# Kernel tuning notes

Hardware: AMD Instinct MI355X
Metric: run time of the kernel (lower is better)

Reference implementation:

```python
import jax, jax.numpy as jnp
import numpy as np

N = 50000      # nodes
E = 800000     # edges (avg degree 16)
C_IN = 256
C_OUT = 256
H = 4
D = C_OUT // H  # 64
NEG_SLOPE = 0.2


def setup_inputs() -> dict:
    key = jax.random.key(0)
    ks = jax.random.split(key, 12)
    glorot = lambda k, shape: jax.random.uniform(k, shape, jnp.float32, -1.0, 1.0) * np.sqrt(6.0 / (shape[0] + shape[1]))
    return {
        "x": jax.random.normal(ks[0], (N, C_IN), jnp.float32),
        "src": jax.random.randint(ks[1], (E,), 0, N, jnp.int32),
        "dst": jax.random.randint(ks[2], (E,), 0, N, jnp.int32),
        "Wl": glorot(ks[3], (C_IN, C_OUT)),
        "bl": jnp.zeros((C_OUT,), jnp.float32),
        "Wr": glorot(ks[4], (C_IN, C_OUT)),
        "br": jnp.zeros((C_OUT,), jnp.float32),
        "Wv": glorot(ks[5], (C_IN, C_OUT)),
        "bv": jnp.zeros((C_OUT,), jnp.float32),
        "att_l": jax.random.normal(ks[6], (1, H, D), jnp.float32) * 0.1,
        "att_r": jax.random.normal(ks[7], (1, H, D), jnp.float32) * 0.1,
    }


def reference(x, src, dst, Wl, bl, Wr, br, Wv, bv, att_l, att_r):
    # lambda_policy=None, gcn_mode=False -> lmbda = lmbda2 = 1.0
    n = x.shape[0]
    sl = ((x @ Wl + bl).reshape(n, H, D) * att_l).sum(-1, keepdims=True)  # [N,H,1]
    sr = ((x @ Wr + br).reshape(n, H, D) * att_r).sum(-1, keepdims=True)  # [N,H,1]
    xv = (x @ Wv + bv).reshape(n, H, D)                                    # [N,H,D]

    # --- convolve branch: average scores over in-neighborhood (incl. self) ---
    hlr = jnp.concatenate([sl, sr], axis=1)                   # [N,2H,1]
    conv = jax.ops.segment_sum(hlr[src], dst, num_segments=n)  # sum_{u->v} hsrc[u]
    deg = jax.ops.segment_sum(jnp.ones((src.shape[0],), x.dtype), dst, num_segments=n)
    agg = (hlr + conv) / (1.0 + deg[:, None, None])            # [N,2H,1]
    sl, sr = agg[:, :H], agg[:, H:]

    # --- edge attention: gather-add-leakyrelu, segment softmax over dst ---
    e = jax.nn.leaky_relu(sl[src] + sr[dst], NEG_SLOPE)        # [E,H,1]
    emax = jax.ops.segment_max(e, dst, num_segments=n)
    emax = jnp.where(jnp.isfinite(emax), emax, 0.0)
    ex = jnp.exp(e - emax[dst])
    denom = jax.ops.segment_sum(ex, dst, num_segments=n)
    a = ex / jnp.maximum(denom[dst], 1e-16)                    # [E,H,1]

    # --- weighted message aggregation ---
    out = jax.ops.segment_sum(xv[src] * a, dst, num_segments=n)  # [N,H,D]
    return out
```

## Files before the change

kernel.cpp:

```cpp
#include <hip/hip_runtime.h>

#define C_IN 256
#define C_OUT 256
#define NH 4
#define HD 64
#define NEG_SLOPE 0.2f

typedef _Float16 half8 __attribute__((ext_vector_type(8)));
typedef _Float16 half4v __attribute__((ext_vector_type(4)));
typedef float floatx4 __attribute__((ext_vector_type(4)));

__global__ void make_eff_w(const float* __restrict__ Wl, const float* __restrict__ Wr,
                           const float* __restrict__ bl, const float* __restrict__ br,
                           const float* __restrict__ attl, const float* __restrict__ attr,
                           float* __restrict__ Ws, float* __restrict__ bs)
{
    int c = blockIdx.x;
    int t = threadIdx.x;
    int h = t >> 6, d = t & 63;
    float al = attl[t], ar = attr[t];
    float vl, vr;
    if (c < C_IN) { vl = Wl[c * C_OUT + t] * al; vr = Wr[c * C_OUT + t] * ar; }
    else          { vl = bl[t] * al;             vr = br[t] * ar; }
#pragma unroll
    for (int off = 32; off >= 1; off >>= 1) {
        vl += __shfl_xor(vl, off, 64);
        vr += __shfl_xor(vr, off, 64);
    }
    if (d == 0) {
        if (c < C_IN) { Ws[c * 8 + h] = vl; Ws[c * 8 + 4 + h] = vr; }
        else          { bs[h] = vl;         bs[4 + h] = vr; }
    }
}

__global__ void transpose_w(const float* __restrict__ Wv, _Float16* __restrict__ WvT)
{
    int idx = blockIdx.x * 256 + threadIdx.x;
    int n = idx >> 8, k = idx & 255;
    WvT[n * 256 + k] = (_Float16)Wv[k * 256 + n];
}

__global__ __launch_bounds__(256) void node_scores(const float* __restrict__ x,
    const float* __restrict__ Ws, const float* __restrict__ bs,
    float* __restrict__ s, int N)
{
    int lane = threadIdx.x & 63, wid = threadIdx.x >> 6;
    float w[4][8];
#pragma unroll
    for (int i = 0; i < 4; ++i)
#pragma unroll
        for (int jq = 0; jq < 2; ++jq) {
            float4 v = *(const float4*)(Ws + (4 * lane + i) * 8 + jq * 4);
            w[i][jq * 4 + 0] = v.x; w[i][jq * 4 + 1] = v.y;
            w[i][jq * 4 + 2] = v.z; w[i][jq * 4 + 3] = v.w;
        }
    float b0[8];
#pragma unroll
    for (int j = 0; j < 8; ++j) b0[j] = bs[j];

    int wglob = blockIdx.x * 4 + wid;
    int nwaves = gridDim.x * 4;
    for (int n = wglob; n < N; n += nwaves) {
        float4 xv4 = *(const float4*)(x + (size_t)n * 256 + 4 * lane);
        float acc[8];
#pragma unroll
        for (int j = 0; j < 8; ++j)
            acc[j] = xv4.x * w[0][j] + xv4.y * w[1][j] + xv4.z * w[2][j] + xv4.w * w[3][j];
#pragma unroll
        for (int off = 32; off >= 1; off >>= 1)
#pragma unroll
            for (int j = 0; j < 8; ++j) acc[j] += __shfl_xor(acc[j], off, 64);
        if (lane == 0) {
            *(float4*)(s + (size_t)n * 8)     = make_float4(acc[0] + b0[0], acc[1] + b0[1], acc[2] + b0[2], acc[3] + b0[3]);
            *(float4*)(s + (size_t)n * 8 + 4) = make_float4(acc[4] + b0[4], acc[5] + b0[5], acc[6] + b0[6], acc[7] + b0[7]);
        }
    }
}

__global__ __launch_bounds__(256) void gemm_xv(const float* __restrict__ x,
    const _Float16* __restrict__ WvT, const float* __restrict__ bv,
    _Float16* __restrict__ xv, int M)
{
    __shared__ __align__(16) _Float16 As[128][40];
    __shared__ __align__(16) _Float16 Bs[128][40];
    int tid = threadIdx.x;
    int wid = tid >> 6, lane = tid & 63;
    int quad = lane >> 4, r16 = lane & 15;
    int m0 = blockIdx.x * 128, n0 = blockIdx.y * 128;

    floatx4 acc[2][8];
#pragma unroll
    for (int i = 0; i < 2; ++i)
#pragma unroll
        for (int j = 0; j < 8; ++j) acc[i][j] = (floatx4){0.f, 0.f, 0.f, 0.f};

    int arow = tid >> 3, af4 = tid & 7;
    int brow = tid >> 2, bg  = tid & 3;

    for (int k0 = 0; k0 < 256; k0 += 32) {
#pragma unroll
        for (int p = 0; p < 4; ++p) {
            int rr = arow + p * 32;
            int gm = m0 + rr;
            float4 v = make_float4(0.f, 0.f, 0.f, 0.f);
            if (gm < M) v = *(const float4*)(x + (size_t)gm * 256 + k0 + af4 * 4);
            _Float16* dp = &As[rr][af4 * 4];
            dp[0] = (_Float16)v.x; dp[1] = (_Float16)v.y;
            dp[2] = (_Float16)v.z; dp[3] = (_Float16)v.w;
        }
#pragma unroll
        for (int p = 0; p < 2; ++p) {
            int nr = brow + p * 64;
            *(float4*)&Bs[nr][bg * 8] = *(const float4*)(WvT + (size_t)(n0 + nr) * 256 + k0 + bg * 8);
        }
        __syncthreads();
        half8 a[2], b[8];
#pragma unroll
        for (int rg = 0; rg < 2; ++rg)
            a[rg] = *(const half8*)&As[wid * 32 + rg * 16 + r16][quad * 8];
#pragma unroll
        for (int cg = 0; cg < 8; ++cg)
            b[cg] = *(const half8*)&Bs[cg * 16 + r16][quad * 8];
#pragma unroll
        for (int rg = 0; rg < 2; ++rg)
#pragma unroll
            for (int cg = 0; cg < 8; ++cg)
                acc[rg][cg] = __builtin_amdgcn_mfma_f32_16x16x32_f16(a[rg], b[cg], acc[rg][cg], 0, 0, 0);
        __syncthreads();
    }
#pragma unroll
    for (int rg = 0; rg < 2; ++rg) {
        int rbase = m0 + wid * 32 + rg * 16 + quad * 4;
#pragma unroll
        for (int cg = 0; cg < 8; ++cg) {
            int gcol = n0 + cg * 16 + r16;
            float bias = bv[gcol];
#pragma unroll
            for (int rr = 0; rr < 4; ++rr) {
                int grow = rbase + rr;
                if (grow < M)
                    xv[(size_t)grow * 256 + gcol] = (_Float16)(acc[rg][cg][rr] + bias);
            }
        }
    }
}

__global__ void deg_kernel(const int* __restrict__ dst, int* __restrict__ deg, int E)
{
    int i = blockIdx.x * 256 + threadIdx.x;
    if (i < E) atomicAdd(&deg[dst[i]], 1);
}

__global__ void scan_part(const int* __restrict__ deg, int* __restrict__ partials,
                          int N, int chunk)
{
    __shared__ int sd[256];
    int b = blockIdx.x, t = threadIdx.x;
    int idx = b * chunk + t;
    int v = (t < chunk && idx < N) ? deg[idx] : 0;
    sd[t] = v; __syncthreads();
    for (int off = 128; off >= 1; off >>= 1) {
        if (t < off) sd[t] += sd[t + off];
        __syncthreads();
    }
    if (t == 0) partials[b] = sd[0];
}

__global__ void scan_partials(const int* __restrict__ partials, int* __restrict__ pscan)
{
    __shared__ int sd[256];
    int t = threadIdx.x;
    int v = partials[t];
    sd[t] = v; __syncthreads();
    for (int off = 1; off < 256; off <<= 1) {
        int x = (t >= off) ? sd[t - off] : 0;
        __syncthreads();
        sd[t] += x;
        __syncthreads();
    }
    pscan[t] = sd[t] - v;
}

__global__ void scan_final(const int* __restrict__ deg, const int* __restrict__ pscan,
                           int* __restrict__ offs, int N, int chunk)
{
    __shared__ int sd[256];
    int b = blockIdx.x, t = threadIdx.x;
    int idx = b * chunk + t;
    int v = (t < chunk && idx < N) ? deg[idx] : 0;
    sd[t] = v; __syncthreads();
    for (int off = 1; off < 256; off <<= 1) {
        int x = (t >= off) ? sd[t - off] : 0;
        __syncthreads();
        sd[t] += x;
        __syncthreads();
    }
    int incl = sd[t], excl = incl - v;
    int base = pscan[b];
    if (t < chunk && idx < N) offs[idx] = base + excl;
    if (idx == N - 1) offs[N] = base + incl;
}

__global__ void scatter_kernel(const int* __restrict__ src, const int* __restrict__ dst,
                               const int* __restrict__ offs, int* __restrict__ cursor,
                               int* __restrict__ csr_src, int E)
{
    int i = blockIdx.x * 256 + threadIdx.x;
    if (i < E) {
        int d = dst[i];
        int p = offs[d] + atomicAdd(&cursor[d], 1);
        csr_src[p] = src[i];
    }
}

__global__ void agg_kernel(const float* __restrict__ s, const int* __restrict__ csr_src,
                           const int* __restrict__ offs, const int* __restrict__ deg,
                           float* __restrict__ aggl, float* __restrict__ aggr, int N)
{
    int gid = blockIdx.x * 256 + threadIdx.x;
    int n = gid >> 3, c = gid & 7;
    if (n >= N) return;
    int off = offs[n], dg = deg[n];
    float acc = s[(size_t)n * 8 + c];
    int i = 0;
    for (; i + 4 <= dg; i += 4) {
        int p0 = csr_src[off + i];
        int p1 = csr_src[off + i + 1];
        int p2 = csr_src[off + i + 2];
        int p3 = csr_src[off + i + 3];
        float v0 = s[(size_t)p0 * 8 + c];
        float v1 = s[(size_t)p1 * 8 + c];
        float v2 = s[(size_t)p2 * 8 + c];
        float v3 = s[(size_t)p3 * 8 + c];
        acc += (v0 + v1) + (v2 + v3);
    }
    for (; i < dg; ++i) acc += s[(size_t)csr_src[off + i] * 8 + c];
    acc *= 1.0f / (1.0f + (float)dg);
    if (c < 4) aggl[(size_t)n * 4 + c]     = acc;
    else       aggr[(size_t)n * 4 + c - 4] = acc;
}

__global__ __launch_bounds__(256) void attn_out(const float* __restrict__ aggl,
    const float* __restrict__ aggr, const int* __restrict__ csr_src,
    const int* __restrict__ offs, const int* __restrict__ deg,
    const _Float16* __restrict__ xv, float* __restrict__ out, int N)
{
    int wid = threadIdx.x >> 6, lane = threadIdx.x & 63;
    int myhead = lane >> 4, myedge = lane & 15, grp = lane & 48;
    int nwaves = gridDim.x * 4;

    for (int n = blockIdx.x * 4 + wid; n < N; n += nwaves) {
        int off = offs[n], dg = deg[n];
        float ar = aggr[(unsigned)(n * 4 + myhead)];

        float denom = 0.f, o0 = 0.f, o1 = 0.f, o2 = 0.f, o3 = 0.f;

        int cs = 0; float wexp = 0.f;
        if (myedge < dg) {
            cs = csr_src[off + myedge];
            float e = aggl[(unsigned)((cs << 2) + myhead)] + ar;
            e = (e > 0.f) ? e : NEG_SLOPE * e;
            wexp = __expf(e);
        }

        for (int b = 0; b < dg; b += 16) {
            int   cs_c = cs;
            float w_c  = wexp;
            cs = 0; wexp = 0.f;
            int nb = b + 16;
            if (nb + myedge < dg) {
                cs = csr_src[off + nb + myedge];
                float e = aggl[(unsigned)((cs << 2) + myhead)] + ar;
                e = (e > 0.f) ? e : NEG_SLOPE * e;
                wexp = __expf(e);
            }
            denom += w_c;
#pragma unroll
            for (int j = 0; j < 16; ++j) {
                int   sidx = __shfl(cs_c, j, 64);
                float w    = __shfl(w_c, grp + j, 64);
                const half4v hv = *(const half4v*)(xv + (unsigned)((sidx << 8) | (lane << 2)));
                o0 += w * (float)hv[0];
                o1 += w * (float)hv[1];
                o2 += w * (float)hv[2];
                o3 += w * (float)hv[3];
            }
        }

#pragma unroll
        for (int o = 1; o <= 8; o <<= 1) denom += __shfl_xor(denom, o, 64);
        float inv = 1.0f / fmaxf(denom, 1e-16f);
        floatx4 res = {o0 * inv, o1 * inv, o2 * inv, o3 * inv};
        __builtin_nontemporal_store(res, (floatx4*)(out + (size_t)n * 256 + (lane << 2)));
    }
}

extern "C" void kernel_launch(void* const* d_in, const int* in_sizes, int n_in,
                              void* d_out, int out_size, void* d_ws, size_t ws_size,
                              hipStream_t stream)
{
    const float* x    = (const float*)d_in[0];
    const int*   src  = (const int*)d_in[1];
    const int*   dst  = (const int*)d_in[2];
    const float* Wl   = (const float*)d_in[3];
    const float* bl   = (const float*)d_in[4];
    const float* Wr   = (const float*)d_in[5];
    const float* br   = (const float*)d_in[6];
    const float* Wv   = (const float*)d_in[7];
    const float* bv   = (const float*)d_in[8];
    const float* attl = (const float*)d_in[9];
    const float* attr = (const float*)d_in[10];
    float* out = (float*)d_out;

    int N = in_sizes[0] / C_IN;
    int E = in_sizes[1];

    char* p = (char*)d_ws;
    auto alloc = [&](size_t bytes) -> void* {
        uintptr_t q = (uintptr_t)p;
        q = (q + 255) & ~(uintptr_t)255;
        p = (char*)(q + bytes);
        return (void*)q;
    };
    float* Ws     = (float*)alloc((size_t)C_IN * 8 * sizeof(float));
    float* bs     = (float*)alloc(8 * sizeof(float));
    float* s      = (float*)alloc((size_t)N * 8 * sizeof(float));
    float* aggl   = (float*)alloc((size_t)N * 4 * sizeof(float));
    float* aggr   = (float*)alloc((size_t)N * 4 * sizeof(float));
    int* deg      = (int*)alloc((size_t)N * sizeof(int));
    int* offs     = (int*)alloc((size_t)(N + 1) * sizeof(int));
    int* cursor   = (int*)alloc((size_t)N * sizeof(int));
    int* partials = (int*)alloc(256 * sizeof(int));
    int* pscan    = (int*)alloc(256 * sizeof(int));
    int* csr_src  = (int*)alloc((size_t)E * sizeof(int));
    _Float16* WvT = (_Float16*)alloc((size_t)C_IN * C_OUT * sizeof(_Float16));
    _Float16* xv  = (_Float16*)alloc((size_t)N * C_OUT * sizeof(_Float16));

    hipMemsetAsync(deg, 0, (size_t)N * sizeof(int), stream);
    hipMemsetAsync(cursor, 0, (size_t)N * sizeof(int), stream);

    make_eff_w<<<C_IN + 1, 256, 0, stream>>>(Wl, Wr, bl, br, attl, attr, Ws, bs);
    transpose_w<<<(C_IN * C_OUT) / 256, 256, 0, stream>>>(Wv, WvT);
    node_scores<<<768, 256, 0, stream>>>(x, Ws, bs, s, N);
    gemm_xv<<<dim3((N + 127) / 128, C_OUT / 128), 256, 0, stream>>>(x, WvT, bv, xv, N);
    deg_kernel<<<(E + 255) / 256, 256, 0, stream>>>(dst, deg, E);
    int chunk = (N + 255) / 256;
    scan_part<<<256, 256, 0, stream>>>(deg, partials, N, chunk);
    scan_partials<<<1, 256, 0, stream>>>(partials, pscan);
    scan_final<<<256, 256, 0, stream>>>(deg, pscan, offs, N, chunk);
    scatter_kernel<<<(E + 255) / 256, 256, 0, stream>>>(src, dst, offs, cursor, csr_src, E);
    agg_kernel<<<(N * 8 + 255) / 256, 256, 0, stream>>>(s, csr_src, offs, deg, aggl, aggr, N);
    attn_out<<<2048, 256, 0, stream>>>(aggl, aggr, csr_src, offs, deg, xv, out, N);
}
```

Before: 351.0 us.

## Split wave into two edge halves with 16-byte xv gathers in attention kernel

The attention/aggregation kernel now has each half-wave process alternating edges, with every lane loading 8 fp16 features (16 bytes) per gather instead of 4. The two halves' partial sums are combined with a cross-half shuffle before the store. The grid-stride loop and next-batch prefetch are replaced by one wave per node launched over N/4 blocks. The GEMM staging also writes the converted fp16 values as one vector store. The aim is wider memory transactions and fewer loop iterations for the gather-bound step, at the cost of losing the software prefetch and issuing a larger grid.

```diff
diff --git a/kernel.cpp b/kernel.cpp
--- a/kernel.cpp
+++ b/kernel.cpp
@@ -104,9 +104,10 @@
             int gm = m0 + rr;
             float4 v = make_float4(0.f, 0.f, 0.f, 0.f);
             if (gm < M) v = *(const float4*)(x + (size_t)gm * 256 + k0 + af4 * 4);
-            _Float16* dp = &As[rr][af4 * 4];
-            dp[0] = (_Float16)v.x; dp[1] = (_Float16)v.y;
-            dp[2] = (_Float16)v.z; dp[3] = (_Float16)v.w;
+            half4v tmp;
+            tmp[0] = (_Float16)v.x; tmp[1] = (_Float16)v.y;
+            tmp[2] = (_Float16)v.z; tmp[3] = (_Float16)v.w;
+            *(half4v*)&As[rr][af4 * 4] = tmp;
         }
 #pragma unroll
         for (int p = 0; p < 2; ++p) {
@@ -246,52 +247,59 @@
     const _Float16* __restrict__ xv, float* __restrict__ out, int N)
 {
     int wid = threadIdx.x >> 6, lane = threadIdx.x & 63;
-    int myhead = lane >> 4, myedge = lane & 15, grp = lane & 48;
-    int nwaves = gridDim.x * 4;
-
-    for (int n = blockIdx.x * 4 + wid; n < N; n += nwaves) {
-        int off = offs[n], dg = deg[n];
-        float ar = aggr[(unsigned)(n * 4 + myhead)];
-
-        float denom = 0.f, o0 = 0.f, o1 = 0.f, o2 = 0.f, o3 = 0.f;
-
+    int n = blockIdx.x * 4 + wid;
+    if (n >= N) return;
+    int myhead = lane >> 4, myedge = lane & 15;
+    int ehalf = lane >> 5;
+    int cgrp  = lane & 31;
+    int wbase = ((lane & 24) << 1) + ehalf;
+    int off = offs[n], dg = deg[n];
+    float ar = aggr[(unsigned)(n * 4 + myhead)];
+
+    float denom = 0.f;
+    float o[8] = {0.f, 0.f, 0.f, 0.f, 0.f, 0.f, 0.f, 0.f};
+
+    for (int b = 0; b < dg; b += 16) {
+        int rem = dg - b;
+        int cnt = rem < 16 ? rem : 16;
         int cs = 0; float wexp = 0.f;
-        if (myedge < dg) {
-            cs = csr_src[off + myedge];
+        if (myedge < cnt) {
+            cs = csr_src[off + b + myedge];
             float e = aggl[(unsigned)((cs << 2) + myhead)] + ar;
             e = (e > 0.f) ? e : NEG_SLOPE * e;
             wexp = __expf(e);
         }
-
-        for (int b = 0; b < dg; b += 16) {
-            int   cs_c = cs;
-            float w_c  = wexp;
-            cs = 0; wexp = 0.f;
-            int nb = b + 16;
-            if (nb + myedge < dg) {
-                cs = csr_src[off + nb + myedge];
-                float e = aggl[(unsigned)((cs << 2) + myhead)] + ar;
-                e = (e > 0.f) ? e : NEG_SLOPE * e;
-                wexp = __expf(e);
+        denom += wexp;
+        if (cnt == 16) {
+#pragma unroll
+            for (int j = 0; j < 16; j += 2) {
+                int   sidx = __shfl(cs, j + ehalf, 64);
+                float w    = __shfl(wexp, wbase + j, 64);
+                const half8 hv = *(const half8*)(xv + (unsigned)((sidx << 8) + (cgrp << 3)));
+#pragma unroll
+                for (int k = 0; k < 8; ++k) o[k] += w * (float)hv[k];
             }
-            denom += w_c;
-#pragma unroll
-            for (int j = 0; j < 16; ++j) {
-                int   sidx = __shfl(cs_c, j, 64);
-                float w    = __shfl(w_c, grp + j, 64);
-                const half4v hv = *(const half4v*)(xv + (unsigned)((sidx << 8) | (lane << 2)));
-                o0 += w * (float)hv[0];
-                o1 += w * (float)hv[1];
-                o2 += w * (float)hv[2];
-                o3 += w * (float)hv[3];
+        } else {
+            for (int j = 0; j < cnt; j += 2) {
+                int   sidx = __shfl(cs, j + ehalf, 64);
+                float w    = __shfl(wexp, wbase + j, 64);
+                const half8 hv = *(const half8*)(xv + (unsigned)((sidx << 8) + (cgrp << 3)));
+#pragma unroll
+                for (int k = 0; k < 8; ++k) o[k] += w * (float)hv[k];
             }
         }
-
-#pragma unroll
-        for (int o = 1; o <= 8; o <<= 1) denom += __shfl_xor(denom, o, 64);
-        float inv = 1.0f / fmaxf(denom, 1e-16f);
-        floatx4 res = {o0 * inv, o1 * inv, o2 * inv, o3 * inv};
-        __builtin_nontemporal_store(res, (floatx4*)(out + (size_t)n * 256 + (lane << 2)));
+    }
+
+#pragma unroll
+    for (int o2 = 1; o2 <= 8; o2 <<= 1) denom += __shfl_xor(denom, o2, 64);
+    float dh = __shfl(denom, ((lane >> 3) & 3) << 4, 64);
+    float inv = 1.0f / fmaxf(dh, 1e-16f);
+#pragma unroll
+    for (int k = 0; k < 8; ++k) { o[k] += __shfl_xor(o[k], 32, 64); o[k] *= inv; }
+    if (lane < 32) {
+        float* op = out + (size_t)n * 256 + (cgrp << 3);
+        *(float4*)op       = make_float4(o[0], o[1], o[2], o[3]);
+        *(float4*)(op + 4) = make_float4(o[4], o[5], o[6], o[7]);
     }
 }
 
@@ -350,5 +358,5 @@
     scan_final<<<256, 256, 0, stream>>>(deg, pscan, offs, N, chunk);
     scatter_kernel<<<(E + 255) / 256, 256, 0, stream>>>(src, dst, offs, cursor, csr_src, E);
     agg_kernel<<<(N * 8 + 255) / 256, 256, 0, stream>>>(s, csr_src, offs, deg, aggl, aggr, N);
-    attn_out<<<2048, 256, 0, stream>>>(aggl, aggr, csr_src, offs, deg, xv, out, N);
-}
+    attn_out<<<(N + 3) / 4, 256, 0, stream>>>(aggl, aggr, csr_src, offs, deg, xv, out, N);
+}
```

New measurement: 350.0 us. Within noise of the previous version (-0.3%).

## Skip padded gathers in attention aggregation and launch one wave per node

Applied to the files above, without the earlier changes.

The attention-output kernel now gathers only as many neighbor rows as the node actually has. It does this by splitting each 16-edge chunk into power-of-two sub-blocks, where before it always ran the full 16 gathers and multiplied the padded ones by zero weight. The grid-stride loop is replaced with one wave per node, and the first 64 edges' indices, scores and exponentials are all loaded up front to raise memory-level parallelism. The GEMM staging also writes the four fp16 values as a single vector store. The trade-off is more branching and register pressure, and more blocks to launch.

```diff
diff --git a/kernel.cpp b/kernel.cpp
--- a/kernel.cpp
+++ b/kernel.cpp
@@ -104,9 +104,10 @@
             int gm = m0 + rr;
             float4 v = make_float4(0.f, 0.f, 0.f, 0.f);
             if (gm < M) v = *(const float4*)(x + (size_t)gm * 256 + k0 + af4 * 4);
-            _Float16* dp = &As[rr][af4 * 4];
-            dp[0] = (_Float16)v.x; dp[1] = (_Float16)v.y;
-            dp[2] = (_Float16)v.z; dp[3] = (_Float16)v.w;
+            half4v tmp;
+            tmp[0] = (_Float16)v.x; tmp[1] = (_Float16)v.y;
+            tmp[2] = (_Float16)v.z; tmp[3] = (_Float16)v.w;
+            *(half4v*)&As[rr][af4 * 4] = tmp;
         }
 #pragma unroll
         for (int p = 0; p < 2; ++p) {
@@ -240,59 +241,100 @@
     else       aggr[(size_t)n * 4 + c - 4] = acc;
 }
 
+template<int SZ>
+__device__ __forceinline__ void gather_sub(int cs, float w, int base, int grp, int lane,
+    const _Float16* __restrict__ xv,
+    float& o0, float& o1, float& o2, float& o3)
+{
+#pragma unroll
+    for (int j = 0; j < SZ; ++j) {
+        int   sidx = __shfl(cs, base + j, 64);
+        float wv   = __shfl(w, grp + base + j, 64);
+        const half4v hv = *(const half4v*)(xv + (unsigned)((sidx << 8) | (lane << 2)));
+        o0 += wv * (float)hv[0];
+        o1 += wv * (float)hv[1];
+        o2 += wv * (float)hv[2];
+        o3 += wv * (float)hv[3];
+    }
+}
+
+__device__ __forceinline__ void do_chunk(int cs, float w, int cnt, int grp, int lane,
+    const _Float16* __restrict__ xv,
+    float& o0, float& o1, float& o2, float& o3)
+{
+    if (cnt == 16) { gather_sub<16>(cs, w, 0, grp, lane, xv, o0, o1, o2, o3); return; }
+    int b = 0;
+    if (cnt & 8) { gather_sub<8>(cs, w, b, grp, lane, xv, o0, o1, o2, o3); b += 8; }
+    if (cnt & 4) { gather_sub<4>(cs, w, b, grp, lane, xv, o0, o1, o2, o3); b += 4; }
+    if (cnt & 2) { gather_sub<2>(cs, w, b, grp, lane, xv, o0, o1, o2, o3); b += 2; }
+    if (cnt & 1) { gather_sub<1>(cs, w, b, grp, lane, xv, o0, o1, o2, o3); }
+}
+
 __global__ __launch_bounds__(256) void attn_out(const float* __restrict__ aggl,
     const float* __restrict__ aggr, const int* __restrict__ csr_src,
     const int* __restrict__ offs, const int* __restrict__ deg,
     const _Float16* __restrict__ xv, float* __restrict__ out, int N)
 {
     int wid = threadIdx.x >> 6, lane = threadIdx.x & 63;
+    int n = blockIdx.x * 4 + wid;
+    if (n >= N) return;
     int myhead = lane >> 4, myedge = lane & 15, grp = lane & 48;
-    int nwaves = gridDim.x * 4;
-
-    for (int n = blockIdx.x * 4 + wid; n < N; n += nwaves) {
-        int off = offs[n], dg = deg[n];
-        float ar = aggr[(unsigned)(n * 4 + myhead)];
-
-        float denom = 0.f, o0 = 0.f, o1 = 0.f, o2 = 0.f, o3 = 0.f;
-
-        int cs = 0; float wexp = 0.f;
-        if (myedge < dg) {
-            cs = csr_src[off + myedge];
+    int off = offs[n], dg = deg[n];
+    const int* cb = csr_src + off;
+    float ar = aggr[(unsigned)(n * 4 + myhead)];
+
+    float o0 = 0.f, o1 = 0.f, o2 = 0.f, o3 = 0.f;
+
+    int cs0 = 0, cs1 = 0, cs2 = 0, cs3 = 0;
+    int e1 = myedge + 16, e2 = myedge + 32, e3 = myedge + 48;
+    if (myedge < dg) cs0 = cb[myedge];
+    if (e1 < dg)     cs1 = cb[e1];
+    if (e2 < dg)     cs2 = cb[e2];
+    if (e3 < dg)     cs3 = cb[e3];
+    float a0 = 0.f, a1 = 0.f, a2 = 0.f, a3 = 0.f;
+    if (myedge < dg) a0 = aggl[(unsigned)((cs0 << 2) + myhead)];
+    if (e1 < dg)     a1 = aggl[(unsigned)((cs1 << 2) + myhead)];
+    if (e2 < dg)     a2 = aggl[(unsigned)((cs2 << 2) + myhead)];
+    if (e3 < dg)     a3 = aggl[(unsigned)((cs3 << 2) + myhead)];
+    float w0 = 0.f, w1 = 0.f, w2 = 0.f, w3 = 0.f;
+    if (myedge < dg) { float e = a0 + ar; e = (e > 0.f) ? e : NEG_SLOPE * e; w0 = __expf(e); }
+    if (e1 < dg)     { float e = a1 + ar; e = (e > 0.f) ? e : NEG_SLOPE * e; w1 = __expf(e); }
+    if (e2 < dg)     { float e = a2 + ar; e = (e > 0.f) ? e : NEG_SLOPE * e; w2 = __expf(e); }
+    if (e3 < dg)     { float e = a3 + ar; e = (e > 0.f) ? e : NEG_SLOPE * e; w3 = __expf(e); }
+    float denom = w0; denom += w1; denom += w2; denom += w3;
+
+    int c0 = dg < 16 ? dg : 16;
+    do_chunk(cs0, w0, c0, grp, lane, xv, o0, o1, o2, o3);
+    if (dg > 16) {
+        int c1 = dg - 16 < 16 ? dg - 16 : 16;
+        do_chunk(cs1, w1, c1, grp, lane, xv, o0, o1, o2, o3);
+    }
+    if (dg > 32) {
+        int c2 = dg - 32 < 16 ? dg - 32 : 16;
+        do_chunk(cs2, w2, c2, grp, lane, xv, o0, o1, o2, o3);
+    }
+    if (dg > 48) {
+        int c3 = dg - 48 < 16 ? dg - 48 : 16;
+        do_chunk(cs3, w3, c3, grp, lane, xv, o0, o1, o2, o3);
+    }
+    for (int b = 64; b < dg; b += 16) {
+        int cs = 0; float w = 0.f;
+        if (b + myedge < dg) {
+            cs = cb[b + myedge];
             float e = aggl[(unsigned)((cs << 2) + myhead)] + ar;
             e = (e > 0.f) ? e : NEG_SLOPE * e;
-            wexp = __expf(e);
-        }
-
-        for (int b = 0; b < dg; b += 16) {
-            int   cs_c = cs;
-            float w_c  = wexp;
-            cs = 0; wexp = 0.f;
-            int nb = b + 16;
-            if (nb + myedge < dg) {
-                cs = csr_src[off + nb + myedge];
-                float e = aggl[(unsigned)((cs << 2) + myhead)] + ar;
-                e = (e > 0.f) ? e : NEG_SLOPE * e;
-                wexp = __expf(e);
-            }
-            denom += w_c;
-#pragma unroll
-            for (int j = 0; j < 16; ++j) {
-                int   sidx = __shfl(cs_c, j, 64);
-                float w    = __shfl(w_c, grp + j, 64);
-                const half4v hv = *(const half4v*)(xv + (unsigned)((sidx << 8) | (lane << 2)));
-                o0 += w * (float)hv[0];
-                o1 += w * (float)hv[1];
-                o2 += w * (float)hv[2];
-                o3 += w * (float)hv[3];
-            }
-        }
-
-#pragma unroll
-        for (int o = 1; o <= 8; o <<= 1) denom += __shfl_xor(denom, o, 64);
-        float inv = 1.0f / fmaxf(denom, 1e-16f);
-        floatx4 res = {o0 * inv, o1 * inv, o2 * inv, o3 * inv};
-        __builtin_nontemporal_store(res, (floatx4*)(out + (size_t)n * 256 + (lane << 2)));
-    }
+            w = __expf(e);
+        }
+        denom += w;
+        int cnt = dg - b < 16 ? dg - b : 16;
+        do_chunk(cs, w, cnt, grp, lane, xv, o0, o1, o2, o3);
+    }
+
+#pragma unroll
+    for (int o = 1; o <= 8; o <<= 1) denom += __shfl_xor(denom, o, 64);
+    float inv = 1.0f / fmaxf(denom, 1e-16f);
+    floatx4 res = {o0 * inv, o1 * inv, o2 * inv, o3 * inv};
+    __builtin_nontemporal_store(res, (floatx4*)(out + (size_t)n * 256 + (lane << 2)));
 }
 
 extern "C" void kernel_launch(void* const* d_in, const int* in_sizes, int n_in,
@@ -350,5 +392,5 @@
     scan_final<<<256, 256, 0, stream>>>(deg, pscan, offs, N, chunk);
     scatter_kernel<<<(E + 255) / 256, 256, 0, stream>>>(src, dst, offs, cursor, csr_src, E);
     agg_kernel<<<(N * 8 + 255) / 256, 256, 0, stream>>>(s, csr_src, offs, deg, aggl, aggr, N);
-    attn_out<<<2048, 256, 0, stream>>>(aggl, aggr, csr_src, offs, deg, xv, out, N);
-}
+    attn_out<<<(N + 3) / 4, 256, 0, stream>>>(aggl, aggr, csr_src, offs, deg, xv, out, N);
+}
```

Result: no change. 344.9 us (-1.7%).
